# Performance work log

Measured on AMD Instinct MI355X. Metric: run time of the kernel, lower is better.

## Reference

```python
import jax, jax.numpy as jnp
import numpy as np

E = 8          # n_experts
TOP_K = 2      # n_active_experts


def setup_inputs() -> dict:
    key = jax.random.key(0)
    ks = jax.random.split(key, 9)
    B, S, D, H = 4, 2048, 2048, 1408
    w = 0.02  # weight scale for numerical stability
    return {
        "x": jax.random.normal(ks[0], (B, S, D), dtype=jnp.float32),
        "gate_w": jax.random.normal(ks[1], (E, D), dtype=jnp.float32) * w,
        "expert_bias": jnp.zeros((E,), dtype=jnp.float32),
        "Wg": jax.random.normal(ks[2], (E, H, D), dtype=jnp.float32) * w,
        "Wu": jax.random.normal(ks[3], (E, H, D), dtype=jnp.float32) * w,
        "Wd": jax.random.normal(ks[4], (E, D, H), dtype=jnp.float32) * w,
        "Ws_g": jax.random.normal(ks[5], (H, D), dtype=jnp.float32) * w,
        "Ws_u": jax.random.normal(ks[6], (H, D), dtype=jnp.float32) * w,
        "Ws_d": jax.random.normal(ks[7], (D, H), dtype=jnp.float32) * w,
    }


def _swiglu(x, wg, wu, wd):
    # torch Linear layout: y = x @ W.T
    return (jax.nn.silu(x @ wg.T) * (x @ wu.T)) @ wd.T


def reference(x, gate_w, expert_bias, Wg, Wu, Wd, Ws_g, Ws_u, Ws_d):
    B, S, D = x.shape
    flat = x.reshape(-1, D)                      # [N, D]
    N = flat.shape[0]

    logits = flat @ gate_w.T                     # [N, E]
    probs = jax.nn.softmax(logits, axis=-1)
    biased = logits + expert_bias
    _, top_idx = jax.lax.top_k(biased, TOP_K)    # [N, K] (bias used only for selection)
    top_w = jnp.take_along_axis(probs, top_idx, axis=-1)
    top_w = top_w / jnp.sum(top_w, axis=-1, keepdims=True)

    # dense per-token combine weights: cw[n, e] = sum_k top_w[n,k] * (top_idx[n,k]==e)
    rows = jnp.arange(N)[:, None]
    cw = jnp.zeros((N, E), dtype=flat.dtype).at[rows, top_idx].add(top_w)

    out = jnp.zeros_like(flat)
    for e in range(E):  # fixed small expert count; equivalent to gather/scatter dispatch
        out = out + cw[:, e:e + 1] * _swiglu(flat, Wg[e], Wu[e], Wd[e])

    out = out + _swiglu(flat, Ws_g, Ws_u, Ws_d)  # shared expert
    return out.reshape(B, S, D)
```

## Files before the change

kernel.cpp:

```cpp
#include <hip/hip_runtime.h>
#include <hip/hip_bf16.h>

#define N_TOK 8192
#define DDIM  2048
#define HDIM  1408
#define ROWS_R 16384
#define ROWS_T 24576
#define MAXTILES 104
#define BM 256
#define BN 128
#define BK 64

typedef unsigned short u16;
typedef unsigned int   u32;
typedef __bf16 bf16x8 __attribute__((ext_vector_type(8)));
typedef float  f32x4  __attribute__((ext_vector_type(4)));

__device__ __forceinline__ u16 f2bf(float f) {
  union { float f; u32 u; } v; v.f = f;
  u32 u = v.u;
  return (u16)((u + 0x7fffu + ((u >> 16) & 1u)) >> 16);
}
__device__ __forceinline__ float bf2f(u16 b) {
  union { u32 u; float f; } v; v.u = ((u32)b) << 16; return v.f;
}

typedef __attribute__((address_space(1))) void gvoid;
typedef __attribute__((address_space(3))) void lvoid;
__device__ __forceinline__ void gload16(const void* g, void* l) {
  __builtin_amdgcn_global_load_lds((gvoid*)g, (lvoid*)l, 16, 0, 0);
}

#define BAR __builtin_amdgcn_s_barrier()
#define SP1 __builtin_amdgcn_s_setprio(1)
#define SP0 __builtin_amdgcn_s_setprio(0)
#define LGK0 do { asm volatile("s_waitcnt lgkmcnt(0)" ::: "memory"); \
                  __builtin_amdgcn_sched_barrier(0); } while (0)
#define VMCNT(n) asm volatile("s_waitcnt vmcnt(" #n ")" ::: "memory")

#define READ_AF(base, mb, dst) { \
  _Pragma("unroll") for (int m_ = 0; m_ < 2; ++m_) { \
    int r_ = ((mb) >> 1) * 128 + wr * 32 + m_ * 16 + l15; \
    _Pragma("unroll") for (int kk_ = 0; kk_ < 2; ++kk_) { \
      int cch_ = kk_ * 4 + lhi; \
      (dst)[m_ * 2 + kk_] = *(const bf16x8*)((const char*)(base) + r_ * 128 + ((cch_ ^ (r_ & 7)) * 16)); } } }

#define READ_BF(base, dst) { \
  _Pragma("unroll") for (int n_ = 0; n_ < 4; ++n_) { \
    int r_ = wc * 64 + n_ * 16 + l15; \
    _Pragma("unroll") for (int kk_ = 0; kk_ < 2; ++kk_) { \
      int cch_ = kk_ * 4 + lhi; \
      (dst)[n_ * 2 + kk_] = *(const bf16x8*)((const char*)(base) + r_ * 128 + ((cch_ ^ (r_ & 7)) * 16)); } } }

#define MFMAQ(AF, BB, ACC, MB) { \
  _Pragma("unroll") for (int m_ = 0; m_ < 2; ++m_) \
  _Pragma("unroll") for (int n_ = 0; n_ < 4; ++n_) \
  _Pragma("unroll") for (int kk_ = 0; kk_ < 2; ++kk_) \
    (ACC)[(MB) + m_][n_] = __builtin_amdgcn_mfma_f32_16x16x32_bf16((AF)[m_ * 2 + kk_], (BB)[n_ * 2 + kk_], (ACC)[(MB) + m_][n_], 0, 0, 0); }

__global__ void k_gate(const float* __restrict__ x, const float* __restrict__ gw,
                       const float* __restrict__ bias, int* __restrict__ tok_idx,
                       float* __restrict__ wts, int* __restrict__ counts,
                       u16* __restrict__ xb) {
  int lane = threadIdx.x & 63;
  int n = blockIdx.x * 4 + (threadIdx.x >> 6);
  const float* xr = x + (size_t)n * DDIM;
  u16* xbr = xb + (size_t)n * DDIM;
  float acc[8];
#pragma unroll
  for (int e = 0; e < 8; ++e) acc[e] = 0.f;
#pragma unroll 2
  for (int j0 = 0; j0 < DDIM; j0 += 256) {
    float4 xv = *(const float4*)(xr + j0 + lane * 4);
    u32 p0 = (u32)f2bf(xv.x) | ((u32)f2bf(xv.y) << 16);
    u32 p1 = (u32)f2bf(xv.z) | ((u32)f2bf(xv.w) << 16);
    *(uint2*)(xbr + j0 + lane * 4) = make_uint2(p0, p1);
#pragma unroll
    for (int e = 0; e < 8; ++e) {
      float4 gv = *(const float4*)(gw + e * DDIM + j0 + lane * 4);
      acc[e] += xv.x * gv.x + xv.y * gv.y + xv.z * gv.z + xv.w * gv.w;
    }
  }
#pragma unroll
  for (int e = 0; e < 8; ++e) {
#pragma unroll
    for (int off = 32; off > 0; off >>= 1) acc[e] += __shfl_xor(acc[e], off);
  }
  if (lane == 0) {
    float m = acc[0];
    for (int e = 1; e < 8; ++e) m = fmaxf(m, acc[e]);
    float p[8];
    for (int e = 0; e < 8; ++e) p[e] = expf(acc[e] - m);
    float b0[8];
    for (int e = 0; e < 8; ++e) b0[e] = acc[e] + bias[e];
    int i0 = 0;
    for (int e = 1; e < 8; ++e) if (b0[e] > b0[i0]) i0 = e;
    int i1 = (i0 == 0) ? 1 : 0;
    for (int e = 0; e < 8; ++e) if (e != i0 && b0[e] > b0[i1]) i1 = e;
    float w0 = p[i0], w1 = p[i1], inv = 1.f / (w0 + w1);
    tok_idx[2 * n] = i0; tok_idx[2 * n + 1] = i1;
    wts[2 * n] = w0 * inv; wts[2 * n + 1] = w1 * inv;
    atomicAdd(&counts[i0], 1); atomicAdd(&counts[i1], 1);
  }
}

__global__ void k_scan(const int* __restrict__ counts, int* __restrict__ offsets,
                       int* __restrict__ cursors, int* __restrict__ ntiles,
                       int4* __restrict__ tiles) {
  if (threadIdx.x != 0 || blockIdx.x != 0) return;
  int off = 0, idx = 0;
  for (int e = 0; e < 8; ++e) {
    offsets[e] = off; cursors[e] = 0;
    int T = counts[e];
    for (int r = 0; r < T; r += BM) {
      int nr = T - r; if (nr > BM) nr = BM;
      tiles[idx++] = make_int4(e, off + r, nr, 0);
    }
    off += T;
  }
  offsets[8] = off;
  for (int r = 0; r < N_TOK; r += BM)
    tiles[idx++] = make_int4(8, ROWS_R + r, BM, 0);
  *ntiles = idx;
}

__global__ void k_build(const int* __restrict__ tok_idx, const int* __restrict__ offsets,
                        int* __restrict__ cursors, int* __restrict__ token_ids,
                        int* __restrict__ pos) {
  int n = blockIdx.x * blockDim.x + threadIdx.x;
  if (n >= N_TOK) return;
#pragma unroll
  for (int s = 0; s < 2; ++s) {
    int e = tok_idx[2 * n + s];
    int p = offsets[e] + atomicAdd(&cursors[e], 1);
    token_ids[p] = n;
    pos[2 * n + s] = p;
  }
  token_ids[ROWS_R + n] = n;
}

__global__ void k_convall(const float* __restrict__ Wg, const float* __restrict__ Wsg,
                          const float* __restrict__ Wu, const float* __restrict__ Wsu,
                          const float* __restrict__ Wd, const float* __restrict__ Wsd,
                          u16* __restrict__ wgb, u16* __restrict__ wub, u16* __restrict__ wdb) {
  const long PER = (long)9 * HDIM * DDIM / 8;
  const long BIG = (long)8 * HDIM * DDIM / 8;
  const long TOT = 3 * PER;
  long stride = (long)gridDim.x * blockDim.x;
  for (long i = (long)blockIdx.x * blockDim.x + threadIdx.x; i < TOT; i += stride) {
    int g = (int)(i / PER);
    long r = i - (long)g * PER;
    const float* src; u16* dst;
    if (g == 0)      { dst = wgb; src = (r < BIG) ? Wg + r * 8 : Wsg + (r - BIG) * 8; }
    else if (g == 1) { dst = wub; src = (r < BIG) ? Wu + r * 8 : Wsu + (r - BIG) * 8; }
    else             { dst = wdb; src = (r < BIG) ? Wd + r * 8 : Wsd + (r - BIG) * 8; }
    float4 a = ((const float4*)src)[0], b = ((const float4*)src)[1];
    u32 p0 = (u32)f2bf(a.x) | ((u32)f2bf(a.y) << 16);
    u32 p1 = (u32)f2bf(a.z) | ((u32)f2bf(a.w) << 16);
    u32 p2 = (u32)f2bf(b.x) | ((u32)f2bf(b.y) << 16);
    u32 p3 = (u32)f2bf(b.z) | ((u32)f2bf(b.w) << 16);
    ((uint4*)dst)[r] = make_uint4(p0, p1, p2, p3);
  }
}

__global__ __launch_bounds__(512, 2) void k_gemm1(
    const u16* __restrict__ xb, const u16* __restrict__ wgb,
    const int* __restrict__ token_ids, const int* __restrict__ ntiles,
    const int4* __restrict__ tiles, u16* __restrict__ h) {
  __shared__ u16 As[2][BM * BK];
  __shared__ u16 Bgs[2][BN * BK];
  __shared__ u16 Bus[2][BN * BK];

  int ntl = *ntiles;
  int nwg = (HDIM / BN) * ntl;
  int bid = blockIdx.x;
  if (bid >= nwg) return;
  int q8 = nwg >> 3, r8 = nwg & 7;
  int xcd = bid & 7, pp = bid >> 3;
  int lid = (xcd < r8 ? xcd * (q8 + 1) : r8 * (q8 + 1) + (xcd - r8) * q8) + pp;
  int bx = lid / ntl, tile = lid - bx * ntl;

  int4 tl = tiles[tile];
  int set = tl.x, grow = tl.y, nrows = tl.z;

  int t = threadIdx.x;
  int wid = t >> 6, lane = t & 63;
  int wr = wid >> 1, wc = wid & 1;
  int l15 = lane & 15, lhi = lane >> 4;

  const u16* aptr[4];
#pragma unroll
  for (int i = 0; i < 4; ++i) {
    int chunk = i * 512 + t;
    int r = chunk >> 3, cc = chunk & 7;
    int c = cc ^ (r & 7);
    int rr = r < nrows ? r : nrows - 1;
    int tok = token_ids[grow + rr];
    aptr[i] = xb + (size_t)tok * DDIM + c * 8;
  }
  const u16* gptr[2];
#pragma unroll
  for (int i = 0; i < 2; ++i) {
    int chunk = i * 512 + t;
    int r = chunk >> 3, cc = chunk & 7;
    int c = cc ^ (r & 7);
    gptr[i] = wgb + (size_t)set * (HDIM * DDIM) + (size_t)(bx * BN + r) * DDIM + c * 8;
  }
  const size_t WUOFF = (size_t)9 * HDIM * DDIM;

#define G1_A0(b, k0) { gload16(aptr[0] + (k0), (char*)As[b] + (size_t)t * 16); \
                       gload16(aptr[1] + (k0), (char*)As[b] + (size_t)(512 + t) * 16); }
#define G1_A1(b, k0) { gload16(aptr[2] + (k0), (char*)As[b] + (size_t)(1024 + t) * 16); \
                       gload16(aptr[3] + (k0), (char*)As[b] + (size_t)(1536 + t) * 16); }
#define G1_BG(b, k0) { gload16(gptr[0] + (k0), (char*)Bgs[b] + (size_t)t * 16); \
                       gload16(gptr[1] + (k0), (char*)Bgs[b] + (size_t)(512 + t) * 16); }
#define G1_BU(b, k0) { gload16(gptr[0] + WUOFF + (k0), (char*)Bus[b] + (size_t)t * 16); \
                       gload16(gptr[1] + WUOFF + (k0), (char*)Bus[b] + (size_t)(512 + t) * 16); }

  f32x4 accg[4][4], accu[4][4];
  f32x4 z = {0.f, 0.f, 0.f, 0.f};
#pragma unroll
  for (int m = 0; m < 4; ++m)
#pragma unroll
    for (int n = 0; n < 4; ++n) { accg[m][n] = z; accu[m][n] = z; }

  const int NK = DDIM / BK;

  VMCNT(0);
  G1_BG(0, 0); G1_A0(0, 0); G1_A1(0, 0); G1_BU(0, 0);
  VMCNT(4); BAR;

  for (int kt = 0; kt < NK - 1; ++kt) {
    int cur = kt & 1, nxt = cur ^ 1;
    int k1 = (kt + 1) * BK;
    bf16x8 a01[4], a23[4], bb[8];
    READ_AF(As[cur], 0, a01);
    READ_BF(Bgs[cur], bb);
    G1_BG(nxt, k1);
    BAR; LGK0;
    SP1; MFMAQ(a01, bb, accg, 0); SP0;
    VMCNT(4); BAR;
    READ_AF(As[cur], 2, a23);
    G1_A0(nxt, k1);
    BAR; LGK0;
    SP1; MFMAQ(a23, bb, accg, 2); SP0;
    VMCNT(4); BAR;
    READ_BF(Bus[cur], bb);
    G1_A1(nxt, k1);
    BAR; LGK0;
    SP1; MFMAQ(a01, bb, accu, 0); SP0;
    BAR;
    G1_BU(nxt, k1);
    BAR;
    SP1; MFMAQ(a23, bb, accu, 2); SP0;
    VMCNT(4); BAR;
  }
  {
    int cur = (NK - 1) & 1;
    VMCNT(0); BAR;
    bf16x8 a01[4], a23[4], bg8[8], bu8[8];
    READ_AF(As[cur], 0, a01);
    READ_AF(As[cur], 2, a23);
    READ_BF(Bgs[cur], bg8);
    READ_BF(Bus[cur], bu8);
    LGK0;
    MFMAQ(a01, bg8, accg, 0); MFMAQ(a23, bg8, accg, 2);
    MFMAQ(a01, bu8, accu, 0); MFMAQ(a23, bu8, accu, 2);
  }

#pragma unroll
  for (int m = 0; m < 4; ++m) {
#pragma unroll
    for (int n = 0; n < 4; ++n) {
      int col = bx * BN + wc * 64 + n * 16 + l15;
#pragma unroll
      for (int qq = 0; qq < 4; ++qq) {
        int rl = (m >> 1) * 128 + wr * 32 + (m & 1) * 16 + lhi * 4 + qq;
        if (rl < nrows) {
          float g = accg[m][n][qq], u = accu[m][n][qq];
          float hv = g / (1.f + expf(-g)) * u;
          h[(size_t)(grow + rl) * HDIM + col] = f2bf(hv);
        }
      }
    }
  }
#undef G1_A0
#undef G1_A1
#undef G1_BG
#undef G1_BU
}

__global__ __launch_bounds__(512, 2) void k_gemm2(
    const u16* __restrict__ h, const u16* __restrict__ wdb,
    const int* __restrict__ ntiles, const int4* __restrict__ tiles,
    u16* __restrict__ y) {
  __shared__ u16 As2[3][BM * BK];
  __shared__ u16 Bs2[3][BN * BK];

  int ntl = *ntiles;
  int nwg = (DDIM / BN) * ntl;
  int bid = blockIdx.x;
  if (bid >= nwg) return;
  int q8 = nwg >> 3, r8 = nwg & 7;
  int xcd = bid & 7, pp = bid >> 3;
  int lid = (xcd < r8 ? xcd * (q8 + 1) : r8 * (q8 + 1) + (xcd - r8) * q8) + pp;
  int bx = lid / ntl, tile = lid - bx * ntl;

  int4 tl = tiles[tile];
  int set = tl.x, grow = tl.y, nrows = tl.z;

  int t = threadIdx.x;
  int wid = t >> 6, lane = t & 63;
  int wr = wid >> 1, wc = wid & 1;
  int l15 = lane & 15, lhi = lane >> 4;

  const u16* aptr[4];
#pragma unroll
  for (int i = 0; i < 4; ++i) {
    int chunk = i * 512 + t;
    int r = chunk >> 3, cc = chunk & 7;
    int c = cc ^ (r & 7);
    aptr[i] = h + (size_t)(grow + r) * HDIM + c * 8;
  }
  const u16* bptr[2];
#pragma unroll
  for (int i = 0; i < 2; ++i) {
    int chunk = i * 512 + t;
    int r = chunk >> 3, cc = chunk & 7;
    int c = cc ^ (r & 7);
    bptr[i] = wdb + (size_t)set * (DDIM * HDIM) + (size_t)(bx * BN + r) * HDIM + c * 8;
  }

#define G2_A(b, k0) { gload16(aptr[0] + (k0), (char*)As2[b] + (size_t)t * 16); \
                      gload16(aptr[1] + (k0), (char*)As2[b] + (size_t)(512 + t) * 16); \
                      gload16(aptr[2] + (k0), (char*)As2[b] + (size_t)(1024 + t) * 16); \
                      gload16(aptr[3] + (k0), (char*)As2[b] + (size_t)(1536 + t) * 16); }
#define G2_B(b, k0) { gload16(bptr[0] + (k0), (char*)Bs2[b] + (size_t)t * 16); \
                      gload16(bptr[1] + (k0), (char*)Bs2[b] + (size_t)(512 + t) * 16); }

  f32x4 acc[4][4];
  f32x4 z = {0.f, 0.f, 0.f, 0.f};
#pragma unroll
  for (int m = 0; m < 4; ++m)
#pragma unroll
    for (int n = 0; n < 4; ++n) acc[m][n] = z;

  const int NK2 = HDIM / BK;

  VMCNT(0);
  G2_A(0, 0); G2_B(0, 0);
  G2_A(1, BK); G2_B(1, BK);
  VMCNT(6); BAR;

  for (int kt = 0; kt < NK2 - 2; ++kt) {
    int cur = kt % 3, nx2 = (kt + 2) % 3;
    int k2 = (kt + 2) * BK;
    bf16x8 a01[4], a23[4], bb[8];
    READ_AF(As2[cur], 0, a01);
    READ_BF(Bs2[cur], bb);
    G2_A(nx2, k2);
    BAR; LGK0;
    SP1; MFMAQ(a01, bb, acc, 0); SP0;
    BAR;
    READ_AF(As2[cur], 2, a23);
    G2_B(nx2, k2);
    BAR; LGK0;
    SP1; MFMAQ(a23, bb, acc, 2); SP0;
    VMCNT(6); BAR;
  }
  VMCNT(0); BAR;
  for (int kt = NK2 - 2; kt < NK2; ++kt) {
    int cur = kt % 3;
    bf16x8 a01[4], a23[4], bb[8];
    READ_AF(As2[cur], 0, a01);
    READ_AF(As2[cur], 2, a23);
    READ_BF(Bs2[cur], bb);
    LGK0;
    MFMAQ(a01, bb, acc, 0); MFMAQ(a23, bb, acc, 2);
  }

#pragma unroll
  for (int m = 0; m < 4; ++m) {
#pragma unroll
    for (int n = 0; n < 4; ++n) {
      int col = bx * BN + wc * 64 + n * 16 + l15;
#pragma unroll
      for (int qq = 0; qq < 4; ++qq) {
        int rl = (m >> 1) * 128 + wr * 32 + (m & 1) * 16 + lhi * 4 + qq;
        if (rl < nrows)
          y[(size_t)(grow + rl) * DDIM + col] = f2bf(acc[m][n][qq]);
      }
    }
  }
#undef G2_A
#undef G2_B
}

__global__ void k_comb(const u16* __restrict__ y, const int* __restrict__ pos,
                       const float* __restrict__ wts, float* __restrict__ out) {
  int n = blockIdx.x;
  int c8 = threadIdx.x;
  int p0 = pos[2 * n], p1 = pos[2 * n + 1];
  float w0 = wts[2 * n], w1 = wts[2 * n + 1];
  uint4 a = ((const uint4*)(y + (size_t)p0 * DDIM))[c8];
  uint4 b = ((const uint4*)(y + (size_t)p1 * DDIM))[c8];
  uint4 c = ((const uint4*)(y + (size_t)(ROWS_R + n) * DDIM))[c8];
  float* o = out + (size_t)n * DDIM + c8 * 8;
#pragma unroll
  for (int j = 0; j < 4; ++j) {
    u32 ua = ((const u32*)&a)[j], ub = ((const u32*)&b)[j], uc = ((const u32*)&c)[j];
    o[2 * j]     = w0 * bf2f((u16)(ua & 0xffff)) + w1 * bf2f((u16)(ub & 0xffff)) + bf2f((u16)(uc & 0xffff));
    o[2 * j + 1] = w0 * bf2f((u16)(ua >> 16))    + w1 * bf2f((u16)(ub >> 16))    + bf2f((u16)(uc >> 16));
  }
}

extern "C" void kernel_launch(void* const* d_in, const int* in_sizes, int n_in,
                              void* d_out, int out_size, void* d_ws, size_t ws_size,
                              hipStream_t stream) {
  const float* x    = (const float*)d_in[0];
  const float* gw   = (const float*)d_in[1];
  const float* bias = (const float*)d_in[2];
  const float* Wg   = (const float*)d_in[3];
  const float* Wu   = (const float*)d_in[4];
  const float* Wd   = (const float*)d_in[5];
  const float* Wsg  = (const float*)d_in[6];
  const float* Wsu  = (const float*)d_in[7];
  const float* Wsd  = (const float*)d_in[8];
  float* out = (float*)d_out;

  char* ws = (char*)d_ws;
  size_t off = 0;
  auto alloc = [&](size_t bytes) -> void* {
    void* p = ws + off;
    off += (bytes + 255) & ~(size_t)255;
    return p;
  };
  u16* xb  = (u16*)alloc((size_t)N_TOK * DDIM * 2);
  u16* wgb = (u16*)alloc((size_t)9 * HDIM * DDIM * 2);
  u16* wub = (u16*)alloc((size_t)9 * HDIM * DDIM * 2);
  u16* wdb = (u16*)alloc((size_t)9 * DDIM * HDIM * 2);
  u16* h   = (u16*)alloc((size_t)ROWS_T * HDIM * 2);
  u16* y   = (u16*)alloc((size_t)ROWS_T * DDIM * 2);
  int*   token_ids = (int*)alloc(ROWS_T * 4);
  int*   tok_idx   = (int*)alloc(N_TOK * 2 * 4);
  int*   pos       = (int*)alloc(N_TOK * 2 * 4);
  float* wts       = (float*)alloc(N_TOK * 2 * 4);
  int*   counts  = (int*)alloc(8 * 4);
  int*   offsets = (int*)alloc(9 * 4);
  int*   cursors = (int*)alloc(8 * 4);
  int*   ntiles  = (int*)alloc(4);
  int4*  tiles   = (int4*)alloc(MAXTILES * 16);

  hipMemsetAsync(counts, 0, 8 * 4, stream);
  k_gate<<<N_TOK / 4, 256, 0, stream>>>(x, gw, bias, tok_idx, wts, counts, xb);
  k_scan<<<1, 64, 0, stream>>>(counts, offsets, cursors, ntiles, tiles);
  k_build<<<(N_TOK + 255) / 256, 256, 0, stream>>>(tok_idx, offsets, cursors, token_ids, pos);

  k_convall<<<4096, 256, 0, stream>>>(Wg, Wsg, Wu, Wsu, Wd, Wsd, wgb, wub, wdb);

  k_gemm1<<<(HDIM / BN) * MAXTILES, 512, 0, stream>>>(xb, wgb, token_ids, ntiles, tiles, h);
  k_gemm2<<<(DDIM / BN) * MAXTILES, 512, 0, stream>>>(h, wdb, ntiles, tiles, y);
  k_comb<<<N_TOK, 256, 0, stream>>>(y, pos, wts, out);
}
```

Baseline: 963.5 us.

## Restructure grouped GEMMs with BK=32, 4-stage LDS pipeline and wider GEMM2 tile

Both grouped GEMM kernels now use a K-step of 32 with a four-buffer LDS ring. Each iteration issues a single batch of async global->LDS loads three stages ahead, then does one read+MFMA body, which replaces the old hand-interleaved multi-barrier schedule. GEMM2 moves to a 256x256 output tile with a 2x4 wave layout and 8x4 accumulators per wave, so B is reused more and there are fewer workgroups. The swizzle is changed to fit 64-byte rows. The trade-off is more accumulator registers in GEMM2, more LDS per block, and twice as many barriers per unit of K, which may cut occupancy or add sync overhead.

```diff
diff --git a/kernel.cpp b/kernel.cpp
--- a/kernel.cpp
+++ b/kernel.cpp
@@ -8,8 +8,7 @@
 #define ROWS_T 24576
 #define MAXTILES 104
 #define BM 256
-#define BN 128
-#define BK 64
+#define BK 32
 
 typedef unsigned short u16;
 typedef unsigned int   u32;
@@ -38,25 +37,7 @@
                   __builtin_amdgcn_sched_barrier(0); } while (0)
 #define VMCNT(n) asm volatile("s_waitcnt vmcnt(" #n ")" ::: "memory")
 
-#define READ_AF(base, mb, dst) { \
-  _Pragma("unroll") for (int m_ = 0; m_ < 2; ++m_) { \
-    int r_ = ((mb) >> 1) * 128 + wr * 32 + m_ * 16 + l15; \
-    _Pragma("unroll") for (int kk_ = 0; kk_ < 2; ++kk_) { \
-      int cch_ = kk_ * 4 + lhi; \
-      (dst)[m_ * 2 + kk_] = *(const bf16x8*)((const char*)(base) + r_ * 128 + ((cch_ ^ (r_ & 7)) * 16)); } } }
-
-#define READ_BF(base, dst) { \
-  _Pragma("unroll") for (int n_ = 0; n_ < 4; ++n_) { \
-    int r_ = wc * 64 + n_ * 16 + l15; \
-    _Pragma("unroll") for (int kk_ = 0; kk_ < 2; ++kk_) { \
-      int cch_ = kk_ * 4 + lhi; \
-      (dst)[n_ * 2 + kk_] = *(const bf16x8*)((const char*)(base) + r_ * 128 + ((cch_ ^ (r_ & 7)) * 16)); } } }
-
-#define MFMAQ(AF, BB, ACC, MB) { \
-  _Pragma("unroll") for (int m_ = 0; m_ < 2; ++m_) \
-  _Pragma("unroll") for (int n_ = 0; n_ < 4; ++n_) \
-  _Pragma("unroll") for (int kk_ = 0; kk_ < 2; ++kk_) \
-    (ACC)[(MB) + m_][n_] = __builtin_amdgcn_mfma_f32_16x16x32_bf16((AF)[m_ * 2 + kk_], (BB)[n_ * 2 + kk_], (ACC)[(MB) + m_][n_], 0, 0, 0); }
+#define FSW(r) ((((r) & 3) ^ (((r) >> 2) & 3)))
 
 __global__ void k_gate(const float* __restrict__ x, const float* __restrict__ gw,
                        const float* __restrict__ bias, int* __restrict__ tok_idx,
@@ -167,12 +148,12 @@
     const u16* __restrict__ xb, const u16* __restrict__ wgb,
     const int* __restrict__ token_ids, const int* __restrict__ ntiles,
     const int4* __restrict__ tiles, u16* __restrict__ h) {
-  __shared__ u16 As[2][BM * BK];
-  __shared__ u16 Bgs[2][BN * BK];
-  __shared__ u16 Bus[2][BN * BK];
+  __shared__ u16 As[4][BM * BK];
+  __shared__ u16 Bgs[4][128 * BK];
+  __shared__ u16 Bus[4][128 * BK];
 
   int ntl = *ntiles;
-  int nwg = (HDIM / BN) * ntl;
+  int nwg = (HDIM / 128) * ntl;
   int bid = blockIdx.x;
   if (bid >= nwg) return;
   int q8 = nwg >> 3, r8 = nwg & 7;
@@ -188,34 +169,55 @@
   int wr = wid >> 1, wc = wid & 1;
   int l15 = lane & 15, lhi = lane >> 4;
 
-  const u16* aptr[4];
-#pragma unroll
-  for (int i = 0; i < 4; ++i) {
+  const u16* aptr[2];
+#pragma unroll
+  for (int i = 0; i < 2; ++i) {
     int chunk = i * 512 + t;
-    int r = chunk >> 3, cc = chunk & 7;
-    int c = cc ^ (r & 7);
+    int r = chunk >> 2, cc = chunk & 3;
+    int c = cc ^ FSW(r);
     int rr = r < nrows ? r : nrows - 1;
     int tok = token_ids[grow + rr];
     aptr[i] = xb + (size_t)tok * DDIM + c * 8;
   }
-  const u16* gptr[2];
-#pragma unroll
-  for (int i = 0; i < 2; ++i) {
-    int chunk = i * 512 + t;
-    int r = chunk >> 3, cc = chunk & 7;
-    int c = cc ^ (r & 7);
-    gptr[i] = wgb + (size_t)set * (HDIM * DDIM) + (size_t)(bx * BN + r) * DDIM + c * 8;
+  const u16* gptr;
+  {
+    int r = t >> 2, cc = t & 3;
+    int c = cc ^ FSW(r);
+    gptr = wgb + (size_t)set * (HDIM * DDIM) + (size_t)(bx * 128 + r) * DDIM + c * 8;
   }
   const size_t WUOFF = (size_t)9 * HDIM * DDIM;
 
-#define G1_A0(b, k0) { gload16(aptr[0] + (k0), (char*)As[b] + (size_t)t * 16); \
-                       gload16(aptr[1] + (k0), (char*)As[b] + (size_t)(512 + t) * 16); }
-#define G1_A1(b, k0) { gload16(aptr[2] + (k0), (char*)As[b] + (size_t)(1024 + t) * 16); \
-                       gload16(aptr[3] + (k0), (char*)As[b] + (size_t)(1536 + t) * 16); }
-#define G1_BG(b, k0) { gload16(gptr[0] + (k0), (char*)Bgs[b] + (size_t)t * 16); \
-                       gload16(gptr[1] + (k0), (char*)Bgs[b] + (size_t)(512 + t) * 16); }
-#define G1_BU(b, k0) { gload16(gptr[0] + WUOFF + (k0), (char*)Bus[b] + (size_t)t * 16); \
-                       gload16(gptr[1] + WUOFF + (k0), (char*)Bus[b] + (size_t)(512 + t) * 16); }
+#define G1_ISSUE(b, k0) { \
+  gload16(aptr[0] + (k0), (char*)As[b] + (size_t)t * 16); \
+  gload16(aptr[1] + (k0), (char*)As[b] + (size_t)(512 + t) * 16); \
+  gload16(gptr + (k0), (char*)Bgs[b] + (size_t)t * 16); \
+  gload16(gptr + WUOFF + (k0), (char*)Bus[b] + (size_t)t * 16); }
+
+#define G1_BODY(b) { \
+  bf16x8 a0[2], a1[2], bg[4], bu[4]; \
+  _Pragma("unroll") for (int n_ = 0; n_ < 4; ++n_) { \
+    int r_ = wc * 64 + n_ * 16 + l15; \
+    int off_ = r_ * 64 + ((lhi ^ FSW(r_)) * 16); \
+    bg[n_] = *(const bf16x8*)((const char*)Bgs[b] + off_); \
+    bu[n_] = *(const bf16x8*)((const char*)Bus[b] + off_); } \
+  _Pragma("unroll") for (int m_ = 0; m_ < 2; ++m_) { \
+    int r_ = wr * 32 + m_ * 16 + l15; \
+    a0[m_] = *(const bf16x8*)((const char*)As[b] + r_ * 64 + ((lhi ^ FSW(r_)) * 16)); } \
+  LGK0; SP1; \
+  _Pragma("unroll") for (int m_ = 0; m_ < 2; ++m_) \
+  _Pragma("unroll") for (int n_ = 0; n_ < 4; ++n_) { \
+    accg[m_][n_] = __builtin_amdgcn_mfma_f32_16x16x32_bf16(a0[m_], bg[n_], accg[m_][n_], 0, 0, 0); \
+    accu[m_][n_] = __builtin_amdgcn_mfma_f32_16x16x32_bf16(a0[m_], bu[n_], accu[m_][n_], 0, 0, 0); } \
+  SP0; \
+  _Pragma("unroll") for (int m_ = 0; m_ < 2; ++m_) { \
+    int r_ = 128 + wr * 32 + m_ * 16 + l15; \
+    a1[m_] = *(const bf16x8*)((const char*)As[b] + r_ * 64 + ((lhi ^ FSW(r_)) * 16)); } \
+  LGK0; SP1; \
+  _Pragma("unroll") for (int m_ = 0; m_ < 2; ++m_) \
+  _Pragma("unroll") for (int n_ = 0; n_ < 4; ++n_) { \
+    accg[2 + m_][n_] = __builtin_amdgcn_mfma_f32_16x16x32_bf16(a1[m_], bg[n_], accg[2 + m_][n_], 0, 0, 0); \
+    accu[2 + m_][n_] = __builtin_amdgcn_mfma_f32_16x16x32_bf16(a1[m_], bu[n_], accu[2 + m_][n_], 0, 0, 0); } \
+  SP0; }
 
   f32x4 accg[4][4], accu[4][4];
   f32x4 z = {0.f, 0.f, 0.f, 0.f};
@@ -227,52 +229,23 @@
   const int NK = DDIM / BK;
 
   VMCNT(0);
-  G1_BG(0, 0); G1_A0(0, 0); G1_A1(0, 0); G1_BU(0, 0);
-  VMCNT(4); BAR;
-
-  for (int kt = 0; kt < NK - 1; ++kt) {
-    int cur = kt & 1, nxt = cur ^ 1;
-    int k1 = (kt + 1) * BK;
-    bf16x8 a01[4], a23[4], bb[8];
-    READ_AF(As[cur], 0, a01);
-    READ_BF(Bgs[cur], bb);
-    G1_BG(nxt, k1);
-    BAR; LGK0;
-    SP1; MFMAQ(a01, bb, accg, 0); SP0;
-    VMCNT(4); BAR;
-    READ_AF(As[cur], 2, a23);
-    G1_A0(nxt, k1);
-    BAR; LGK0;
-    SP1; MFMAQ(a23, bb, accg, 2); SP0;
-    VMCNT(4); BAR;
-    READ_BF(Bus[cur], bb);
-    G1_A1(nxt, k1);
-    BAR; LGK0;
-    SP1; MFMAQ(a01, bb, accu, 0); SP0;
-    BAR;
-    G1_BU(nxt, k1);
-    BAR;
-    SP1; MFMAQ(a23, bb, accu, 2); SP0;
-    VMCNT(4); BAR;
-  }
-  {
-    int cur = (NK - 1) & 1;
-    VMCNT(0); BAR;
-    bf16x8 a01[4], a23[4], bg8[8], bu8[8];
-    READ_AF(As[cur], 0, a01);
-    READ_AF(As[cur], 2, a23);
-    READ_BF(Bgs[cur], bg8);
-    READ_BF(Bus[cur], bu8);
-    LGK0;
-    MFMAQ(a01, bg8, accg, 0); MFMAQ(a23, bg8, accg, 2);
-    MFMAQ(a01, bu8, accu, 0); MFMAQ(a23, bu8, accu, 2);
-  }
+  G1_ISSUE(0, 0); G1_ISSUE(1, BK); G1_ISSUE(2, 2 * BK);
+  VMCNT(8); BAR;
+
+  for (int kt = 0; kt < NK - 3; ++kt) {
+    G1_ISSUE((kt + 3) & 3, (kt + 3) * BK);
+    G1_BODY(kt & 3);
+    VMCNT(8); BAR;
+  }
+  G1_BODY((NK - 3) & 3); VMCNT(4); BAR;
+  G1_BODY((NK - 2) & 3); VMCNT(0); BAR;
+  G1_BODY((NK - 1) & 3);
 
 #pragma unroll
   for (int m = 0; m < 4; ++m) {
 #pragma unroll
     for (int n = 0; n < 4; ++n) {
-      int col = bx * BN + wc * 64 + n * 16 + l15;
+      int col = bx * 128 + wc * 64 + n * 16 + l15;
 #pragma unroll
       for (int qq = 0; qq < 4; ++qq) {
         int rl = (m >> 1) * 128 + wr * 32 + (m & 1) * 16 + lhi * 4 + qq;
@@ -284,21 +257,19 @@
       }
     }
   }
-#undef G1_A0
-#undef G1_A1
-#undef G1_BG
-#undef G1_BU
+#undef G1_ISSUE
+#undef G1_BODY
 }
 
 __global__ __launch_bounds__(512, 2) void k_gemm2(
     const u16* __restrict__ h, const u16* __restrict__ wdb,
     const int* __restrict__ ntiles, const int4* __restrict__ tiles,
     u16* __restrict__ y) {
-  __shared__ u16 As2[3][BM * BK];
-  __shared__ u16 Bs2[3][BN * BK];
+  __shared__ u16 As2[4][BM * BK];
+  __shared__ u16 Bs2[4][256 * BK];
 
   int ntl = *ntiles;
-  int nwg = (DDIM / BN) * ntl;
+  int nwg = (DDIM / 256) * ntl;
   int bid = blockIdx.x;
   if (bid >= nwg) return;
   int q8 = nwg >> 3, r8 = nwg & 7;
@@ -311,89 +282,85 @@
 
   int t = threadIdx.x;
   int wid = t >> 6, lane = t & 63;
-  int wr = wid >> 1, wc = wid & 1;
+  int wr = wid >> 2, wc = wid & 3;
   int l15 = lane & 15, lhi = lane >> 4;
 
-  const u16* aptr[4];
-#pragma unroll
-  for (int i = 0; i < 4; ++i) {
-    int chunk = i * 512 + t;
-    int r = chunk >> 3, cc = chunk & 7;
-    int c = cc ^ (r & 7);
-    aptr[i] = h + (size_t)(grow + r) * HDIM + c * 8;
-  }
+  const u16* aptr[2];
   const u16* bptr[2];
 #pragma unroll
   for (int i = 0; i < 2; ++i) {
     int chunk = i * 512 + t;
-    int r = chunk >> 3, cc = chunk & 7;
-    int c = cc ^ (r & 7);
-    bptr[i] = wdb + (size_t)set * (DDIM * HDIM) + (size_t)(bx * BN + r) * HDIM + c * 8;
-  }
-
-#define G2_A(b, k0) { gload16(aptr[0] + (k0), (char*)As2[b] + (size_t)t * 16); \
-                      gload16(aptr[1] + (k0), (char*)As2[b] + (size_t)(512 + t) * 16); \
-                      gload16(aptr[2] + (k0), (char*)As2[b] + (size_t)(1024 + t) * 16); \
-                      gload16(aptr[3] + (k0), (char*)As2[b] + (size_t)(1536 + t) * 16); }
-#define G2_B(b, k0) { gload16(bptr[0] + (k0), (char*)Bs2[b] + (size_t)t * 16); \
-                      gload16(bptr[1] + (k0), (char*)Bs2[b] + (size_t)(512 + t) * 16); }
-
-  f32x4 acc[4][4];
+    int r = chunk >> 2, cc = chunk & 3;
+    int c = cc ^ FSW(r);
+    aptr[i] = h + (size_t)(grow + r) * HDIM + c * 8;
+    bptr[i] = wdb + (size_t)set * (DDIM * HDIM) + (size_t)(bx * 256 + r) * HDIM + c * 8;
+  }
+
+#define G2_ISSUE(b, k0) { \
+  gload16(aptr[0] + (k0), (char*)As2[b] + (size_t)t * 16); \
+  gload16(aptr[1] + (k0), (char*)As2[b] + (size_t)(512 + t) * 16); \
+  gload16(bptr[0] + (k0), (char*)Bs2[b] + (size_t)t * 16); \
+  gload16(bptr[1] + (k0), (char*)Bs2[b] + (size_t)(512 + t) * 16); }
+
+#define G2_BODY(b) { \
+  bf16x8 af[4], bf[4]; \
+  _Pragma("unroll") for (int n_ = 0; n_ < 4; ++n_) { \
+    int r_ = wc * 64 + n_ * 16 + l15; \
+    bf[n_] = *(const bf16x8*)((const char*)Bs2[b] + r_ * 64 + ((lhi ^ FSW(r_)) * 16)); } \
+  _Pragma("unroll") for (int m_ = 0; m_ < 4; ++m_) { \
+    int r_ = wr * 128 + m_ * 16 + l15; \
+    af[m_] = *(const bf16x8*)((const char*)As2[b] + r_ * 64 + ((lhi ^ FSW(r_)) * 16)); } \
+  LGK0; SP1; \
+  _Pragma("unroll") for (int m_ = 0; m_ < 4; ++m_) \
+  _Pragma("unroll") for (int n_ = 0; n_ < 4; ++n_) \
+    acc[m_][n_] = __builtin_amdgcn_mfma_f32_16x16x32_bf16(af[m_], bf[n_], acc[m_][n_], 0, 0, 0); \
+  SP0; \
+  _Pragma("unroll") for (int m_ = 0; m_ < 4; ++m_) { \
+    int r_ = wr * 128 + (4 + m_) * 16 + l15; \
+    af[m_] = *(const bf16x8*)((const char*)As2[b] + r_ * 64 + ((lhi ^ FSW(r_)) * 16)); } \
+  LGK0; SP1; \
+  _Pragma("unroll") for (int m_ = 0; m_ < 4; ++m_) \
+  _Pragma("unroll") for (int n_ = 0; n_ < 4; ++n_) \
+    acc[4 + m_][n_] = __builtin_amdgcn_mfma_f32_16x16x32_bf16(af[m_], bf[n_], acc[4 + m_][n_], 0, 0, 0); \
+  SP0; }
+
+  f32x4 acc[8][4];
   f32x4 z = {0.f, 0.f, 0.f, 0.f};
 #pragma unroll
-  for (int m = 0; m < 4; ++m)
+  for (int m = 0; m < 8; ++m)
 #pragma unroll
     for (int n = 0; n < 4; ++n) acc[m][n] = z;
 
   const int NK2 = HDIM / BK;
 
   VMCNT(0);
-  G2_A(0, 0); G2_B(0, 0);
-  G2_A(1, BK); G2_B(1, BK);
-  VMCNT(6); BAR;
-
-  for (int kt = 0; kt < NK2 - 2; ++kt) {
-    int cur = kt % 3, nx2 = (kt + 2) % 3;
-    int k2 = (kt + 2) * BK;
-    bf16x8 a01[4], a23[4], bb[8];
-    READ_AF(As2[cur], 0, a01);
-    READ_BF(Bs2[cur], bb);
-    G2_A(nx2, k2);
-    BAR; LGK0;
-    SP1; MFMAQ(a01, bb, acc, 0); SP0;
-    BAR;
-    READ_AF(As2[cur], 2, a23);
-    G2_B(nx2, k2);
-    BAR; LGK0;
-    SP1; MFMAQ(a23, bb, acc, 2); SP0;
-    VMCNT(6); BAR;
-  }
-  VMCNT(0); BAR;
-  for (int kt = NK2 - 2; kt < NK2; ++kt) {
-    int cur = kt % 3;
-    bf16x8 a01[4], a23[4], bb[8];
-    READ_AF(As2[cur], 0, a01);
-    READ_AF(As2[cur], 2, a23);
-    READ_BF(Bs2[cur], bb);
-    LGK0;
-    MFMAQ(a01, bb, acc, 0); MFMAQ(a23, bb, acc, 2);
-  }
-
-#pragma unroll
-  for (int m = 0; m < 4; ++m) {
+  G2_ISSUE(0, 0); G2_ISSUE(1, BK); G2_ISSUE(2, 2 * BK);
+  VMCNT(8); BAR;
+
+  for (int kt = 0; kt < NK2 - 3; ++kt) {
+    G2_ISSUE((kt + 3) & 3, (kt + 3) * BK);
+    G2_BODY(kt & 3);
+    VMCNT(8); BAR;
+  }
+  G2_BODY((NK2 - 3) & 3); VMCNT(4); BAR;
+  G2_BODY((NK2 - 2) & 3); VMCNT(0); BAR;
+  G2_BODY((NK2 - 1) & 3);
+
+#pragma unroll
+  for (int m = 0; m < 8; ++m) {
 #pragma unroll
     for (int n = 0; n < 4; ++n) {
-      int col = bx * BN + wc * 64 + n * 16 + l15;
+      int col = bx * 256 + wc * 64 + n * 16 + l15;
 #pragma unroll
       for (int qq = 0; qq < 4; ++qq) {
-        int rl = (m >> 1) * 128 + wr * 32 + (m & 1) * 16 + lhi * 4 + qq;
+        int rl = wr * 128 + m * 16 + lhi * 4 + qq;
         if (rl < nrows)
           y[(size_t)(grow + rl) * DDIM + col] = f2bf(acc[m][n][qq]);
       }
     }
   }
-#undef G2_A
-#undef G2_B
+#undef G2_ISSUE
+#undef G2_BODY
 }
 
 __global__ void k_comb(const u16* __restrict__ y, const int* __restrict__ pos,
@@ -458,7 +425,7 @@
 
   k_convall<<<4096, 256, 0, stream>>>(Wg, Wsg, Wu, Wsu, Wd, Wsd, wgb, wub, wdb);
 
-  k_gemm1<<<(HDIM / BN) * MAXTILES, 512, 0, stream>>>(xb, wgb, token_ids, ntiles, tiles, h);
-  k_gemm2<<<(DDIM / BN) * MAXTILES, 512, 0, stream>>>(h, wdb, ntiles, tiles, y);
+  k_gemm1<<<(HDIM / 128) * MAXTILES, 512, 0, stream>>>(xb, wgb, token_ids, ntiles, tiles, h);
+  k_gemm2<<<(DDIM / 256) * MAXTILES, 512, 0, stream>>>(h, wdb, ntiles, tiles, y);
   k_comb<<<N_TOK, 256, 0, stream>>>(y, pos, wts, out);
 }
```

Result: slower. 1.084 ms (+12.5%).

## Restructure both GEMMs to 256x256 tiles with interleaved gate/up weight rows

Applied to the files above, without the earlier changes.

gemm1 now loads gate and up weight rows interleaved in 16-row groups into one 256-row B tile. Each warp (2x4 warp grid) then holds matching gate/up accumulators and computes SiLU*up locally. gemm2 widens its N tile to 256 and goes from a triple buffer to a double buffer, with a new warp layout and per-warp 128x64 sub-tiles. This raises arithmetic intensity per LDS byte and halves the number of A reloads, at the cost of more accumulator registers, fewer workgroups and a shallower prefetch with full vmcnt(0) waits each iteration.

```diff
diff --git a/kernel.cpp b/kernel.cpp
--- a/kernel.cpp
+++ b/kernel.cpp
@@ -8,7 +8,6 @@
 #define ROWS_T 24576
 #define MAXTILES 104
 #define BM 256
-#define BN 128
 #define BK 64
 
 typedef unsigned short u16;
@@ -38,25 +37,26 @@
                   __builtin_amdgcn_sched_barrier(0); } while (0)
 #define VMCNT(n) asm volatile("s_waitcnt vmcnt(" #n ")" ::: "memory")
 
-#define READ_AF(base, mb, dst) { \
-  _Pragma("unroll") for (int m_ = 0; m_ < 2; ++m_) { \
-    int r_ = ((mb) >> 1) * 128 + wr * 32 + m_ * 16 + l15; \
+#define READ_A8(base, mb) { \
+  _Pragma("unroll") for (int m_ = 0; m_ < 4; ++m_) { \
+    int r_ = wr * 128 + ((mb) + m_) * 16 + l15; \
     _Pragma("unroll") for (int kk_ = 0; kk_ < 2; ++kk_) { \
       int cch_ = kk_ * 4 + lhi; \
-      (dst)[m_ * 2 + kk_] = *(const bf16x8*)((const char*)(base) + r_ * 128 + ((cch_ ^ (r_ & 7)) * 16)); } } }
-
-#define READ_BF(base, dst) { \
-  _Pragma("unroll") for (int n_ = 0; n_ < 4; ++n_) { \
-    int r_ = wc * 64 + n_ * 16 + l15; \
+      af[m_ * 2 + kk_] = *(const bf16x8*)((const char*)(base) + r_ * 128 + ((cch_ ^ (r_ & 7)) * 16)); } } }
+
+#define READ_B4(base, nb) { \
+  _Pragma("unroll") for (int n_ = 0; n_ < 2; ++n_) { \
+    int r_ = wc * 64 + ((nb) + n_) * 16 + l15; \
     _Pragma("unroll") for (int kk_ = 0; kk_ < 2; ++kk_) { \
       int cch_ = kk_ * 4 + lhi; \
-      (dst)[n_ * 2 + kk_] = *(const bf16x8*)((const char*)(base) + r_ * 128 + ((cch_ ^ (r_ & 7)) * 16)); } } }
-
-#define MFMAQ(AF, BB, ACC, MB) { \
-  _Pragma("unroll") for (int m_ = 0; m_ < 2; ++m_) \
-  _Pragma("unroll") for (int n_ = 0; n_ < 4; ++n_) \
+      bf[((nb) + n_) * 2 + kk_] = *(const bf16x8*)((const char*)(base) + r_ * 128 + ((cch_ ^ (r_ & 7)) * 16)); } } }
+
+#define MM16(mb, nb) { \
+  _Pragma("unroll") for (int m_ = 0; m_ < 4; ++m_) \
+  _Pragma("unroll") for (int n_ = 0; n_ < 2; ++n_) \
   _Pragma("unroll") for (int kk_ = 0; kk_ < 2; ++kk_) \
-    (ACC)[(MB) + m_][n_] = __builtin_amdgcn_mfma_f32_16x16x32_bf16((AF)[m_ * 2 + kk_], (BB)[n_ * 2 + kk_], (ACC)[(MB) + m_][n_], 0, 0, 0); }
+    acc[(mb) + m_][(nb) + n_] = __builtin_amdgcn_mfma_f32_16x16x32_bf16( \
+        af[m_ * 2 + kk_], bf[((nb) + n_) * 2 + kk_], acc[(mb) + m_][(nb) + n_], 0, 0, 0); }
 
 __global__ void k_gate(const float* __restrict__ x, const float* __restrict__ gw,
                        const float* __restrict__ bias, int* __restrict__ tok_idx,
@@ -164,15 +164,14 @@
 }
 
 __global__ __launch_bounds__(512, 2) void k_gemm1(
-    const u16* __restrict__ xb, const u16* __restrict__ wgb,
+    const u16* __restrict__ xb, const u16* __restrict__ wgb, const u16* __restrict__ wub,
     const int* __restrict__ token_ids, const int* __restrict__ ntiles,
     const int4* __restrict__ tiles, u16* __restrict__ h) {
   __shared__ u16 As[2][BM * BK];
-  __shared__ u16 Bgs[2][BN * BK];
-  __shared__ u16 Bus[2][BN * BK];
+  __shared__ u16 Bs[2][BM * BK];
 
   int ntl = *ntiles;
-  int nwg = (HDIM / BN) * ntl;
+  int nwg = (HDIM / 128) * ntl;
   int bid = blockIdx.x;
   if (bid >= nwg) return;
   int q8 = nwg >> 3, r8 = nwg & 7;
@@ -185,7 +184,7 @@
 
   int t = threadIdx.x;
   int wid = t >> 6, lane = t & 63;
-  int wr = wid >> 1, wc = wid & 1;
+  int wr = wid >> 2, wc = wid & 3;
   int l15 = lane & 15, lhi = lane >> 4;
 
   const u16* aptr[4];
@@ -198,107 +197,98 @@
     int tok = token_ids[grow + rr];
     aptr[i] = xb + (size_t)tok * DDIM + c * 8;
   }
-  const u16* gptr[2];
-#pragma unroll
-  for (int i = 0; i < 2; ++i) {
+  const u16* bptr[4];
+#pragma unroll
+  for (int i = 0; i < 4; ++i) {
     int chunk = i * 512 + t;
     int r = chunk >> 3, cc = chunk & 7;
     int c = cc ^ (r & 7);
-    gptr[i] = wgb + (size_t)set * (HDIM * DDIM) + (size_t)(bx * BN + r) * DDIM + c * 8;
-  }
-  const size_t WUOFF = (size_t)9 * HDIM * DDIM;
-
-#define G1_A0(b, k0) { gload16(aptr[0] + (k0), (char*)As[b] + (size_t)t * 16); \
-                       gload16(aptr[1] + (k0), (char*)As[b] + (size_t)(512 + t) * 16); }
-#define G1_A1(b, k0) { gload16(aptr[2] + (k0), (char*)As[b] + (size_t)(1024 + t) * 16); \
-                       gload16(aptr[3] + (k0), (char*)As[b] + (size_t)(1536 + t) * 16); }
-#define G1_BG(b, k0) { gload16(gptr[0] + (k0), (char*)Bgs[b] + (size_t)t * 16); \
-                       gload16(gptr[1] + (k0), (char*)Bgs[b] + (size_t)(512 + t) * 16); }
-#define G1_BU(b, k0) { gload16(gptr[0] + WUOFF + (k0), (char*)Bus[b] + (size_t)t * 16); \
-                       gload16(gptr[1] + WUOFF + (k0), (char*)Bus[b] + (size_t)(512 + t) * 16); }
-
-  f32x4 accg[4][4], accu[4][4];
+    int group = r >> 4;
+    int wrow = bx * 128 + (group >> 1) * 16 + (r & 15);
+    const u16* base = (group & 1) ? wub : wgb;
+    bptr[i] = base + (size_t)set * (HDIM * DDIM) + (size_t)wrow * DDIM + c * 8;
+  }
+
+#define ISSUE_A0(b, k0) { gload16(aptr[0] + (k0), (char*)As[b] + (size_t)t * 16); \
+                          gload16(aptr[1] + (k0), (char*)As[b] + (size_t)(512 + t) * 16); }
+#define ISSUE_A1(b, k0) { gload16(aptr[2] + (k0), (char*)As[b] + (size_t)(1024 + t) * 16); \
+                          gload16(aptr[3] + (k0), (char*)As[b] + (size_t)(1536 + t) * 16); }
+#define ISSUE_B0(b, k0) { gload16(bptr[0] + (k0), (char*)Bs[b] + (size_t)t * 16); \
+                          gload16(bptr[1] + (k0), (char*)Bs[b] + (size_t)(512 + t) * 16); }
+#define ISSUE_B1(b, k0) { gload16(bptr[2] + (k0), (char*)Bs[b] + (size_t)(1024 + t) * 16); \
+                          gload16(bptr[3] + (k0), (char*)Bs[b] + (size_t)(1536 + t) * 16); }
+
+  f32x4 acc[8][4];
   f32x4 z = {0.f, 0.f, 0.f, 0.f};
 #pragma unroll
-  for (int m = 0; m < 4; ++m)
-#pragma unroll
-    for (int n = 0; n < 4; ++n) { accg[m][n] = z; accu[m][n] = z; }
-
+  for (int m = 0; m < 8; ++m)
+#pragma unroll
+    for (int n = 0; n < 4; ++n) acc[m][n] = z;
+
+  bf16x8 af[8], bf[8];
   const int NK = DDIM / BK;
 
   VMCNT(0);
-  G1_BG(0, 0); G1_A0(0, 0); G1_A1(0, 0); G1_BU(0, 0);
-  VMCNT(4); BAR;
+  ISSUE_A0(0, 0); ISSUE_A1(0, 0); ISSUE_B0(0, 0); ISSUE_B1(0, 0);
+  VMCNT(0); BAR;
 
   for (int kt = 0; kt < NK - 1; ++kt) {
     int cur = kt & 1, nxt = cur ^ 1;
     int k1 = (kt + 1) * BK;
-    bf16x8 a01[4], a23[4], bb[8];
-    READ_AF(As[cur], 0, a01);
-    READ_BF(Bgs[cur], bb);
-    G1_BG(nxt, k1);
-    BAR; LGK0;
-    SP1; MFMAQ(a01, bb, accg, 0); SP0;
-    VMCNT(4); BAR;
-    READ_AF(As[cur], 2, a23);
-    G1_A0(nxt, k1);
-    BAR; LGK0;
-    SP1; MFMAQ(a23, bb, accg, 2); SP0;
-    VMCNT(4); BAR;
-    READ_BF(Bus[cur], bb);
-    G1_A1(nxt, k1);
-    BAR; LGK0;
-    SP1; MFMAQ(a01, bb, accu, 0); SP0;
-    BAR;
-    G1_BU(nxt, k1);
-    BAR;
-    SP1; MFMAQ(a23, bb, accu, 2); SP0;
-    VMCNT(4); BAR;
+    READ_A8(As[cur], 0); READ_B4(Bs[cur], 0);
+    ISSUE_A0(nxt, k1); ISSUE_B0(nxt, k1);
+    BAR; LGK0;
+    SP1; MM16(0, 0); SP0; BAR;
+    READ_B4(Bs[cur], 2);
+    ISSUE_A1(nxt, k1); ISSUE_B1(nxt, k1);
+    BAR; LGK0;
+    SP1; MM16(0, 2); SP0; BAR;
+    READ_A8(As[cur], 4);
+    BAR; LGK0;
+    SP1; MM16(4, 0); MM16(4, 2); SP0;
+    VMCNT(0); BAR;
   }
   {
     int cur = (NK - 1) & 1;
-    VMCNT(0); BAR;
-    bf16x8 a01[4], a23[4], bg8[8], bu8[8];
-    READ_AF(As[cur], 0, a01);
-    READ_AF(As[cur], 2, a23);
-    READ_BF(Bgs[cur], bg8);
-    READ_BF(Bus[cur], bu8);
+    READ_A8(As[cur], 0); READ_B4(Bs[cur], 0); READ_B4(Bs[cur], 2);
     LGK0;
-    MFMAQ(a01, bg8, accg, 0); MFMAQ(a23, bg8, accg, 2);
-    MFMAQ(a01, bu8, accu, 0); MFMAQ(a23, bu8, accu, 2);
-  }
-
-#pragma unroll
-  for (int m = 0; m < 4; ++m) {
-#pragma unroll
-    for (int n = 0; n < 4; ++n) {
-      int col = bx * BN + wc * 64 + n * 16 + l15;
+    SP1; MM16(0, 0); MM16(0, 2); SP0;
+    READ_A8(As[cur], 4);
+    LGK0;
+    SP1; MM16(4, 0); MM16(4, 2); SP0;
+  }
+
+#pragma unroll
+  for (int m = 0; m < 8; ++m) {
+#pragma unroll
+    for (int j = 0; j < 2; ++j) {
+      int col = bx * 128 + (wc * 2 + j) * 16 + l15;
 #pragma unroll
       for (int qq = 0; qq < 4; ++qq) {
-        int rl = (m >> 1) * 128 + wr * 32 + (m & 1) * 16 + lhi * 4 + qq;
+        int rl = wr * 128 + m * 16 + lhi * 4 + qq;
         if (rl < nrows) {
-          float g = accg[m][n][qq], u = accu[m][n][qq];
+          float g = acc[m][2 * j][qq], u = acc[m][2 * j + 1][qq];
           float hv = g / (1.f + expf(-g)) * u;
           h[(size_t)(grow + rl) * HDIM + col] = f2bf(hv);
         }
       }
     }
   }
-#undef G1_A0
-#undef G1_A1
-#undef G1_BG
-#undef G1_BU
+#undef ISSUE_A0
+#undef ISSUE_A1
+#undef ISSUE_B0
+#undef ISSUE_B1
 }
 
 __global__ __launch_bounds__(512, 2) void k_gemm2(
     const u16* __restrict__ h, const u16* __restrict__ wdb,
     const int* __restrict__ ntiles, const int4* __restrict__ tiles,
     u16* __restrict__ y) {
-  __shared__ u16 As2[3][BM * BK];
-  __shared__ u16 Bs2[3][BN * BK];
+  __shared__ u16 As[2][BM * BK];
+  __shared__ u16 Bs[2][BM * BK];
 
   int ntl = *ntiles;
-  int nwg = (DDIM / BN) * ntl;
+  int nwg = (DDIM / 256) * ntl;
   int bid = blockIdx.x;
   if (bid >= nwg) return;
   int q8 = nwg >> 3, r8 = nwg & 7;
@@ -311,89 +301,86 @@
 
   int t = threadIdx.x;
   int wid = t >> 6, lane = t & 63;
-  int wr = wid >> 1, wc = wid & 1;
+  int wr = wid >> 2, wc = wid & 3;
   int l15 = lane & 15, lhi = lane >> 4;
 
   const u16* aptr[4];
+  const u16* bptr[4];
 #pragma unroll
   for (int i = 0; i < 4; ++i) {
     int chunk = i * 512 + t;
     int r = chunk >> 3, cc = chunk & 7;
     int c = cc ^ (r & 7);
     aptr[i] = h + (size_t)(grow + r) * HDIM + c * 8;
-  }
-  const u16* bptr[2];
-#pragma unroll
-  for (int i = 0; i < 2; ++i) {
-    int chunk = i * 512 + t;
-    int r = chunk >> 3, cc = chunk & 7;
-    int c = cc ^ (r & 7);
-    bptr[i] = wdb + (size_t)set * (DDIM * HDIM) + (size_t)(bx * BN + r) * HDIM + c * 8;
-  }
-
-#define G2_A(b, k0) { gload16(aptr[0] + (k0), (char*)As2[b] + (size_t)t * 16); \
-                      gload16(aptr[1] + (k0), (char*)As2[b] + (size_t)(512 + t) * 16); \
-                      gload16(aptr[2] + (k0), (char*)As2[b] + (size_t)(1024 + t) * 16); \
-                      gload16(aptr[3] + (k0), (char*)As2[b] + (size_t)(1536 + t) * 16); }
-#define G2_B(b, k0) { gload16(bptr[0] + (k0), (char*)Bs2[b] + (size_t)t * 16); \
-                      gload16(bptr[1] + (k0), (char*)Bs2[b] + (size_t)(512 + t) * 16); }
-
-  f32x4 acc[4][4];
+    bptr[i] = wdb + (size_t)set * (DDIM * HDIM) + (size_t)(bx * 256 + r) * HDIM + c * 8;
+  }
+
+#define ISSUE_A0(b, k0) { gload16(aptr[0] + (k0), (char*)As[b] + (size_t)t * 16); \
+                          gload16(aptr[1] + (k0), (char*)As[b] + (size_t)(512 + t) * 16); }
+#define ISSUE_A1(b, k0) { gload16(aptr[2] + (k0), (char*)As[b] + (size_t)(1024 + t) * 16); \
+                          gload16(aptr[3] + (k0), (char*)As[b] + (size_t)(1536 + t) * 16); }
+#define ISSUE_B0(b, k0) { gload16(bptr[0] + (k0), (char*)Bs[b] + (size_t)t * 16); \
+                          gload16(bptr[1] + (k0), (char*)Bs[b] + (size_t)(512 + t) * 16); }
+#define ISSUE_B1(b, k0) { gload16(bptr[2] + (k0), (char*)Bs[b] + (size_t)(1024 + t) * 16); \
+                          gload16(bptr[3] + (k0), (char*)Bs[b] + (size_t)(1536 + t) * 16); }
+
+  f32x4 acc[8][4];
   f32x4 z = {0.f, 0.f, 0.f, 0.f};
 #pragma unroll
-  for (int m = 0; m < 4; ++m)
+  for (int m = 0; m < 8; ++m)
 #pragma unroll
     for (int n = 0; n < 4; ++n) acc[m][n] = z;
 
+  bf16x8 af[8], bf[8];
   const int NK2 = HDIM / BK;
 
   VMCNT(0);
-  G2_A(0, 0); G2_B(0, 0);
-  G2_A(1, BK); G2_B(1, BK);
-  VMCNT(6); BAR;
-
-  for (int kt = 0; kt < NK2 - 2; ++kt) {
-    int cur = kt % 3, nx2 = (kt + 2) % 3;
-    int k2 = (kt + 2) * BK;
-    bf16x8 a01[4], a23[4], bb[8];
-    READ_AF(As2[cur], 0, a01);
-    READ_BF(Bs2[cur], bb);
-    G2_A(nx2, k2);
-    BAR; LGK0;
-    SP1; MFMAQ(a01, bb, acc, 0); SP0;
-    BAR;
-    READ_AF(As2[cur], 2, a23);
-    G2_B(nx2, k2);
-    BAR; LGK0;
-    SP1; MFMAQ(a23, bb, acc, 2); SP0;
-    VMCNT(6); BAR;
-  }
+  ISSUE_A0(0, 0); ISSUE_A1(0, 0); ISSUE_B0(0, 0); ISSUE_B1(0, 0);
   VMCNT(0); BAR;
-  for (int kt = NK2 - 2; kt < NK2; ++kt) {
-    int cur = kt % 3;
-    bf16x8 a01[4], a23[4], bb[8];
-    READ_AF(As2[cur], 0, a01);
-    READ_AF(As2[cur], 2, a23);
-    READ_BF(Bs2[cur], bb);
+
+  for (int kt = 0; kt < NK2 - 1; ++kt) {
+    int cur = kt & 1, nxt = cur ^ 1;
+    int k1 = (kt + 1) * BK;
+    READ_A8(As[cur], 0); READ_B4(Bs[cur], 0);
+    ISSUE_A0(nxt, k1); ISSUE_B0(nxt, k1);
+    BAR; LGK0;
+    SP1; MM16(0, 0); SP0; BAR;
+    READ_B4(Bs[cur], 2);
+    ISSUE_A1(nxt, k1); ISSUE_B1(nxt, k1);
+    BAR; LGK0;
+    SP1; MM16(0, 2); SP0; BAR;
+    READ_A8(As[cur], 4);
+    BAR; LGK0;
+    SP1; MM16(4, 0); MM16(4, 2); SP0;
+    VMCNT(0); BAR;
+  }
+  {
+    int cur = (NK2 - 1) & 1;
+    READ_A8(As[cur], 0); READ_B4(Bs[cur], 0); READ_B4(Bs[cur], 2);
     LGK0;
-    MFMAQ(a01, bb, acc, 0); MFMAQ(a23, bb, acc, 2);
-  }
-
-#pragma unroll
-  for (int m = 0; m < 4; ++m) {
+    SP1; MM16(0, 0); MM16(0, 2); SP0;
+    READ_A8(As[cur], 4);
+    LGK0;
+    SP1; MM16(4, 0); MM16(4, 2); SP0;
+  }
+
+#pragma unroll
+  for (int m = 0; m < 8; ++m) {
 #pragma unroll
     for (int n = 0; n < 4; ++n) {
-      int col = bx * BN + wc * 64 + n * 16 + l15;
+      int col = bx * 256 + wc * 64 + n * 16 + l15;
 #pragma unroll
       for (int qq = 0; qq < 4; ++qq) {
-        int rl = (m >> 1) * 128 + wr * 32 + (m & 1) * 16 + lhi * 4 + qq;
+        int rl = wr * 128 + m * 16 + lhi * 4 + qq;
         if (rl < nrows)
           y[(size_t)(grow + rl) * DDIM + col] = f2bf(acc[m][n][qq]);
       }
     }
   }
-#undef G2_A
-#undef G2_B
+#undef ISSUE_A0
+#undef ISSUE_A1
+#undef ISSUE_B0
+#undef ISSUE_B1
 }
 
 __global__ void k_comb(const u16* __restrict__ y, const int* __restrict__ pos,
@@ -458,7 +445,7 @@
 
   k_convall<<<4096, 256, 0, stream>>>(Wg, Wsg, Wu, Wsu, Wd, Wsd, wgb, wub, wdb);
 
-  k_gemm1<<<(HDIM / BN) * MAXTILES, 512, 0, stream>>>(xb, wgb, token_ids, ntiles, tiles, h);
-  k_gemm2<<<(DDIM / BN) * MAXTILES, 512, 0, stream>>>(h, wdb, ntiles, tiles, y);
+  k_gemm1<<<(HDIM / 128) * MAXTILES, 512, 0, stream>>>(xb, wgb, wub, token_ids, ntiles, tiles, h);
+  k_gemm2<<<(DDIM / 256) * MAXTILES, 512, 0, stream>>>(h, wdb, ntiles, tiles, y);
   k_comb<<<N_TOK, 256, 0, stream>>>(y, pos, wts, out);
 }
```

New measurement: 948.0 us. Within noise of the previous version (-1.6%).
